# Kernel tuning notes

Hardware: AMD Instinct MI355X
Metric: run time of the kernel (lower is better)

The kernel has to match this reference:

```python
import jax, jax.numpy as jnp
from jax import lax
import numpy as np

N, C, D, KNN = 32768, 1000, 1024, 16
EPS_EUC = 1e-12
EPS_COS = 1e-8
COS_THRESH = 0.85


def setup_inputs() -> dict:
    key = jax.random.key(0)
    k1, k2, k3 = jax.random.split(key, 3)
    feature = jax.random.normal(k1, (N, D), dtype=jnp.float32)
    pred = jax.random.normal(k2, (N, C), dtype=jnp.float32)
    unlabeled_index = jnp.arange(N, dtype=jnp.int64) if jax.config.jax_enable_x64 else jnp.arange(N, dtype=jnp.int32)
    # module state: centroids (from FeaturePool), top-N score buffer (init -1), fake index buffer (init -1)
    centroids = jax.random.normal(k3, (C, D), dtype=jnp.float32)
    pred_top_N = jnp.full((C, KNN), -1.0, dtype=jnp.float32)
    fake_index = jnp.full((C, KNN), -1, dtype=jnp.int32)
    return {"feature": feature, "pred": pred, "unlabeled_index": unlabeled_index,
            "centroids": centroids, "pred_top_N": pred_top_N, "fake_index": fake_index}


def reference(feature, pred, unlabeled_index, centroids, pred_top_N, fake_index):
    xx = jnp.sum(feature * feature, axis=1, keepdims=True)          # [N,1]
    yy = jnp.sum(centroids * centroids, axis=1)[None, :]            # [1,C]
    euc = jnp.sqrt(jnp.clip(xx + yy - 2.0 * (feature @ centroids.T), EPS_EUC, None))
    euc_id = jnp.argmin(euc, axis=1)                                # [N]

    scores = jnp.max(jax.nn.softmax(pred, axis=1), axis=1)          # [N] max softmax prob

    # cosine similarity of every sample to every centroid [N, C]
    f_n = feature / jnp.clip(jnp.linalg.norm(feature, axis=1, keepdims=True), EPS_COS, None)
    c_n = centroids / jnp.clip(jnp.linalg.norm(centroids, axis=1, keepdims=True), EPS_COS, None)
    cos = f_n @ c_n.T
    label_idx = jnp.argmax(cos, axis=1)                             # [N]
    cos_max = jnp.max(cos, axis=1)                                  # [N]

    # label[i] = label_idx if (cos-argmax == euc-argmin and cos_max > 0.85) else -1
    label = jnp.where((label_idx == euc_id) & (cos_max > COS_THRESH),
                      label_idx.astype(jnp.float32), -1.0)

    # sequential bounded top-N scatter update of (pred_top_N, fake_index)
    def step(carry, x):
        ptn, fidx = carry
        li, sc, ui = x
        row = ptn[li]                        # [KNN]
        mi = jnp.argmin(row)
        upd = sc > row[mi]
        ptn = ptn.at[li, mi].set(jnp.where(upd, sc, row[mi]))
        fidx = fidx.at[li, mi].set(jnp.where(upd, ui.astype(fidx.dtype), fidx[li, mi]))
        return (ptn, fidx), None

    (ptn_new, fidx_new), _ = lax.scan(step, (pred_top_N, fake_index),
                                      (label_idx, scores, unlabeled_index))
    return label, ptn_new, fidx_new
```

## Files before the change

kernel.cpp:

```cpp
#include <hip/hip_runtime.h>
#include <hip/hip_bf16.h>
#include <math.h>

#define NS 32768
#define NC 1000
#define CP 1024
#define DD 1024
#define KN 16

typedef __attribute__((ext_vector_type(8))) short bf16x8;
typedef __attribute__((ext_vector_type(4))) float f32x4;
typedef __attribute__((ext_vector_type(4))) float float4v;
typedef __attribute__((ext_vector_type(4))) int int4v;
typedef __attribute__((ext_vector_type(8))) unsigned short u16x8;
typedef __attribute__((ext_vector_type(4))) unsigned short u16x4;

__device__ __forceinline__ unsigned short f2bf(float f) {
  unsigned u = __float_as_uint(f);
  u += 0x7FFFu + ((u >> 16) & 1u);
  return (unsigned short)(u >> 16);
}
__device__ __forceinline__ float bf2f(unsigned short h) {
  return __uint_as_float(((unsigned)h) << 16);
}

#define GLL16(g, l) __builtin_amdgcn_global_load_lds( \
    (const __attribute__((address_space(1))) void*)(g), \
    (__attribute__((address_space(3))) void*)(l), 16, 0, 0)

#define PREP_FEAT_BLKS (NS * DD / 4 / 1024)
__global__ __launch_bounds__(256) void k_prep(
    const float* __restrict__ Cm, unsigned short* __restrict__ Cb,
    float* __restrict__ cnorm2, float* __restrict__ invc,
    const float* __restrict__ A, unsigned short* __restrict__ Ab,
    const float* __restrict__ P, float* __restrict__ scores) {
  __shared__ float red[4];
  __shared__ float wmax[4];
  __shared__ double wsum[4];
  int b = blockIdx.x, tid = threadIdx.x;
  int lane = tid & 63, wid = tid >> 6;
  if (b < NS) {
    const float* row = P + (size_t)b * NC;
    bool act = tid < 250;
    float p0 = 0, p1 = 0, p2 = 0, p3 = 0, mx = -1e30f;
    if (act) {
      float4v v = *(const float4v*)(row + tid * 4);
      p0 = v[0]; p1 = v[1]; p2 = v[2]; p3 = v[3];
      mx = fmaxf(fmaxf(p0, p1), fmaxf(p2, p3));
    }
    for (int off = 32; off; off >>= 1) mx = fmaxf(mx, __shfl_xor(mx, off));
    if (!lane) wmax[wid] = mx;
    __syncthreads();
    float m = fmaxf(fmaxf(wmax[0], wmax[1]), fmaxf(wmax[2], wmax[3]));
    double s = 0.0;
    if (act)
      s = (double)__expf(p0 - m) + (double)__expf(p1 - m) +
          (double)__expf(p2 - m) + (double)__expf(p3 - m);
    for (int off = 32; off; off >>= 1) s += __shfl_xor(s, off);
    if (!lane) wsum[wid] = s;
    __syncthreads();
    if (!tid) scores[b] = (float)(1.0 / (wsum[0] + wsum[1] + wsum[2] + wsum[3]));
  } else if (b < NS + PREP_FEAT_BLKS) {
    int bb = b - NS;
    const float4v* src = (const float4v*)A;
    u16x4* dst = (u16x4*)Ab;
#pragma unroll
    for (int r = 0; r < 4; ++r) {
      size_t f = (size_t)bb * 1024 + r * 256 + tid;
      float4v v = src[f];
      u16x4 o = { f2bf(v[0]), f2bf(v[1]), f2bf(v[2]), f2bf(v[3]) };
      dst[f] = o;
    }
  } else {
    int c = b - NS - PREP_FEAT_BLKS;
    float sq = 0.f;
    if (c < NC) {
      float4v v = ((const float4v*)(Cm + (size_t)c * DD))[tid];
      sq = v[0]*v[0] + v[1]*v[1] + v[2]*v[2] + v[3]*v[3];
      u16x4 o = { f2bf(v[0]), f2bf(v[1]), f2bf(v[2]), f2bf(v[3]) };
      *(u16x4*)(Cb + (size_t)c * DD + tid * 4) = o;
    } else {
      u16x4 z = { 0, 0, 0, 0 };
      *(u16x4*)(Cb + (size_t)c * DD + tid * 4) = z;
    }
    for (int off = 32; off; off >>= 1) sq += __shfl_xor(sq, off);
    if (!lane) red[wid] = sq;
    __syncthreads();
    if (!tid) {
      float s = red[0] + red[1] + red[2] + red[3];
      cnorm2[c] = s;
      float n = sqrtf(s); if (n < 1e-8f) n = 1e-8f;
      invc[c] = (c < NC) ? 1.0f / n : 0.0f;
    }
  }
}

#define MF(a_, b_, c_) __builtin_amdgcn_mfma_f32_16x16x32_bf16(a_, b_, c_, 0, 0, 0)
#define RD(base_, i_) (*(const bf16x8*)((base_) + (i_) * 1024 + aoff))
#define SA(s_, b_) do { \
    GLL16(pA0 + (s_) * 32, ldsB + (b_) * 16384 + dA0); \
    GLL16(pA1 + (s_) * 32, ldsB + (b_) * 16384 + dA1); } while (0)
#define SB(s_, b_) do { \
    GLL16(pB0 + (s_) * 32, ldsB + 65536 + (b_) * 16384 + dA0); \
    GLL16(pB1 + (s_) * 32, ldsB + 65536 + (b_) * 16384 + dA1); } while (0)
#define VM4 asm volatile("s_waitcnt vmcnt(4)" ::: "memory")
#define VM0 asm volatile("s_waitcnt vmcnt(0)" ::: "memory")
#define MFMAC(A0_, A1_, A2_, A3_, M0) do { \
    acc[M0+0][0] = MF(A0_, bv0, acc[M0+0][0]); \
    acc[M0+0][1] = MF(A0_, bv1, acc[M0+0][1]); \
    acc[M0+0][2] = MF(A0_, bv2, acc[M0+0][2]); \
    acc[M0+0][3] = MF(A0_, bv3, acc[M0+0][3]); \
    acc[M0+1][0] = MF(A1_, bv0, acc[M0+1][0]); \
    acc[M0+1][1] = MF(A1_, bv1, acc[M0+1][1]); \
    acc[M0+1][2] = MF(A1_, bv2, acc[M0+1][2]); \
    acc[M0+1][3] = MF(A1_, bv3, acc[M0+1][3]); \
    acc[M0+2][0] = MF(A2_, bv0, acc[M0+2][0]); \
    acc[M0+2][1] = MF(A2_, bv1, acc[M0+2][1]); \
    acc[M0+2][2] = MF(A2_, bv2, acc[M0+2][2]); \
    acc[M0+2][3] = MF(A2_, bv3, acc[M0+2][3]); \
    acc[M0+3][0] = MF(A3_, bv0, acc[M0+3][0]); \
    acc[M0+3][1] = MF(A3_, bv1, acc[M0+3][1]); \
    acc[M0+3][2] = MF(A3_, bv2, acc[M0+3][2]); \
    acc[M0+3][3] = MF(A3_, bv3, acc[M0+3][3]); } while (0)
#define KSTEP(s_, STAGE_, GATE_) do { \
    const char* Ab_ = ldsB + ((s_) & 3) * 16384 + wrOff; \
    const char* Bb_ = ldsB + 65536 + ((s_) & 3) * 16384 + wcOff; \
    af0 = RD(Ab_, 0); af1 = RD(Ab_, 1); af2 = RD(Ab_, 2); af3 = RD(Ab_, 3); \
    bv0 = RD(Bb_, 0); bv1 = RD(Bb_, 1); bv2 = RD(Bb_, 2); bv3 = RD(Bb_, 3); \
    af4 = RD(Ab_, 4); af5 = RD(Ab_, 5); af6 = RD(Ab_, 6); af7 = RD(Ab_, 7); \
    STAGE_; \
    __builtin_amdgcn_s_setprio(1); \
    MFMAC(af0, af1, af2, af3, 0); \
    MFMAC(af4, af5, af6, af7, 4); \
    __builtin_amdgcn_s_setprio(0); \
    GATE_; \
    __builtin_amdgcn_s_barrier(); \
  } while (0)

__global__ __launch_bounds__(512, 1) void k_gemm(
    const unsigned short* __restrict__ A,
    const unsigned short* __restrict__ B,
    unsigned short* __restrict__ Dout) {
  __shared__ unsigned short lds[65536];
  char* ldsB = (char*)lds;
  int tid = threadIdx.x, lane = tid & 63, wid = tid >> 6;
  int wr = wid >> 2, wc = wid & 3;
  int bid = (blockIdx.x & 7) * 64 + (blockIdx.x >> 3);
  int cb = bid & 3, rb = bid >> 2;
  int brow = rb * 256, bcol = cb * 256;

  f32x4 acc[8][4];
#pragma unroll
  for (int m = 0; m < 8; ++m)
#pragma unroll
    for (int n = 0; n < 4; ++n) acc[m][n] = (f32x4){0.f, 0.f, 0.f, 0.f};

  int f0 = wid * 64 + lane, f1 = f0 + 512;
  int gl0 = (f0 & 3) ^ ((f0 >> 3) & 3);
  int gl1 = (f1 & 3) ^ ((f1 >> 3) & 3);
  const unsigned short* pA0 = A + (size_t)(brow + (f0 >> 2)) * DD + gl0 * 8;
  const unsigned short* pA1 = A + (size_t)(brow + (f1 >> 2)) * DD + gl1 * 8;
  const unsigned short* pB0 = B + (size_t)(bcol + (f0 >> 2)) * DD + gl0 * 8;
  const unsigned short* pB1 = B + (size_t)(bcol + (f1 >> 2)) * DD + gl1 * 8;
  int dA0 = f0 * 16, dA1 = f1 * 16;

  int aoff = (lane & 15) * 64 + (((lane >> 4) ^ ((lane >> 1) & 3)) * 16);
  int wrOff = wr * 8192;
  int wcOff = wc * 4096;

  bf16x8 af0, af1, af2, af3, af4, af5, af6, af7, bv0, bv1, bv2, bv3;

  SA(0, 0); SB(0, 0);
  SA(1, 1); SB(1, 1);
  VM4;
  __builtin_amdgcn_s_barrier();

  for (int s = 0; s < 30; ++s) {
    int bn = (s + 2) & 3;
    KSTEP(s, { SA(s + 2, bn); SB(s + 2, bn); }, VM4);
  }
  KSTEP(30, (void)0, VM0);
  KSTEP(31, (void)0, (void)0);

  int colb = bcol + wc * 64 + (lane & 15);
  int rowb = brow + wr * 128 + ((lane >> 4) << 2);
#pragma unroll
  for (int m = 0; m < 8; ++m)
#pragma unroll
    for (int n = 0; n < 4; ++n)
#pragma unroll
      for (int j = 0; j < 4; ++j)
        Dout[(size_t)(rowb + m * 16 + j) * CP + colb + n * 16] = f2bf(acc[m][n][j]);
}

__global__ __launch_bounds__(256) void k_argmax(
    const unsigned short* __restrict__ Dot, const float* __restrict__ invc,
    const float* __restrict__ cnorm2, const float* __restrict__ feat,
    const float* __restrict__ cent, float* __restrict__ label_out,
    int* __restrict__ lidx) {
  int tid = threadIdx.x;
  int lane = tid & 63, wid = tid >> 6;
  int i = blockIdx.x * 4 + wid;
  const unsigned short* drow = Dot + (size_t)i * CP;

  float v[2][8];
  float dmax = -1e30f; int darg = CP;
  float emin = 1e30f;  int earg = CP;
#pragma unroll
  for (int it = 0; it < 2; ++it) {
    int c0 = it * 512 + lane * 8;
    bf16x8 d8 = *(const bf16x8*)(drow + c0);
    float4v i0 = *(const float4v*)(invc + c0);
    float4v i1 = *(const float4v*)(invc + c0 + 4);
    float4v n0 = *(const float4v*)(cnorm2 + c0);
    float4v n1 = *(const float4v*)(cnorm2 + c0 + 4);
#pragma unroll
    for (int j = 0; j < 8; ++j) {
      int c = c0 + j;
      float inv = (j < 4) ? i0[j] : i1[j - 4];
      float cn  = (j < 4) ? n0[j] : n1[j - 4];
      float d = bf2f((unsigned short)d8[j]);
      float val, ev;
      if (c < NC) { val = d * inv; ev = cn - 2.0f * d; }
      else        { val = -1e30f;  ev = 1e30f; }
      v[it][j] = val;
      if (val > dmax) { dmax = val; darg = c; }
      if (ev < emin)  { emin = ev;  earg = c; }
    }
  }
  for (int off = 32; off; off >>= 1) {
    float om = __shfl_xor(dmax, off); int oi = __shfl_xor(darg, off);
    if (om > dmax || (om == dmax && oi < darg)) { dmax = om; darg = oi; }
    float oe = __shfl_xor(emin, off); int oj = __shfl_xor(earg, off);
    if (oe < emin || (oe == emin && oj < earg)) { emin = oe; earg = oj; }
  }
  const float MARGIN = 0.15f;
  unsigned long long cmask[2][8]; int ccnt = 0;
#pragma unroll
  for (int it = 0; it < 2; ++it)
#pragma unroll
    for (int j = 0; j < 8; ++j) {
      int c = it * 512 + lane * 8 + j;
      bool cand = (c < NC) && (v[it][j] >= dmax - MARGIN);
      cmask[it][j] = __ballot(cand);
      ccnt += __popcll(cmask[it][j]);
    }
  int finalArg = darg;
  double cosmax_d = -2.0;
  bool need = (ccnt > 1) || (dmax > 10.0f);
  if (need) {
    float xv[16]; double sx = 0.0;
    const float* xr = feat + (size_t)i * DD;
#pragma unroll
    for (int t = 0; t < 16; ++t) {
      float x = xr[t * 64 + lane]; xv[t] = x; sx += (double)x * (double)x;
    }
    for (int off = 32; off; off >>= 1) sx += __shfl_xor(sx, off);
    double nx = sqrt(sx); if (nx < 1e-8) nx = 1e-8;
    double best = -2.0; int besti = CP;
#pragma unroll
    for (int it = 0; it < 2; ++it)
#pragma unroll
      for (int j = 0; j < 8; ++j) {
        unsigned long long mk = cmask[it][j];
        while (mk) {
          int b = __builtin_ctzll(mk); mk &= mk - 1;
          int c = it * 512 + b * 8 + j;
          const float* cr = cent + (size_t)c * DD;
          double s = 0.0, s2 = 0.0;
#pragma unroll
          for (int t = 0; t < 16; ++t) {
            double cv = (double)cr[t * 64 + lane];
            s += (double)xv[t] * cv; s2 += cv * cv;
          }
          for (int off = 32; off; off >>= 1) {
            s += __shfl_xor(s, off); s2 += __shfl_xor(s2, off);
          }
          double nc = sqrt(s2); if (nc < 1e-8) nc = 1e-8;
          double cs = s / (nx * nc);
          if (cs > best || (cs == best && c < besti)) { best = cs; besti = c; }
        }
      }
    finalArg = besti; cosmax_d = best;
  }
  if (!lane) {
    lidx[i] = finalArg;
    float lab = -1.0f;
    if (need && finalArg == earg && cosmax_d > 0.85) lab = (float)finalArg;
    label_out[i] = lab;
  }
}

__global__ __launch_bounds__(64) void k_scan(
    const int* __restrict__ lidx, const float* __restrict__ scores,
    const int* __restrict__ uidx, const float* __restrict__ ptn_in,
    const int* __restrict__ fidx_in, float* __restrict__ out_ptn,
    float* __restrict__ out_fidx) {
  int c = blockIdx.x;
  int lane = threadIdx.x;
  float row[KN]; int idx[KN];
#pragma unroll
  for (int j = 0; j < KN; ++j) {
    row[j] = ptn_in[c * KN + j];
    idx[j] = fidx_in[c * KN + j];
  }
  for (int base = 0; base < NS; base += 256) {
    int l0 = lidx[base + lane];
    int l1 = lidx[base + 64 + lane];
    int l2 = lidx[base + 128 + lane];
    int l3 = lidx[base + 192 + lane];
#pragma unroll
    for (int q = 0; q < 4; ++q) {
      int lab = (q == 0) ? l0 : (q == 1) ? l1 : (q == 2) ? l2 : l3;
      unsigned long long m = __ballot(lab == c);
      while (m) {
        int b = __builtin_ctzll(m); m &= m - 1;
        int i = base + q * 64 + b;
        float s = scores[i];
        int ui = uidx[i];
        int mi = 0; float mn = row[0];
#pragma unroll
        for (int t = 1; t < KN; ++t)
          if (row[t] < mn) { mn = row[t]; mi = t; }
        if (s > mn) {
#pragma unroll
          for (int t = 0; t < KN; ++t)
            if (t == mi) { row[t] = s; idx[t] = ui; }
        }
      }
    }
  }
  if (!lane) {
#pragma unroll
    for (int j = 0; j < KN; ++j) {
      out_ptn[c * KN + j] = row[j];
      out_fidx[c * KN + j] = (float)idx[j];
    }
  }
}

extern "C" void kernel_launch(void* const* d_in, const int* in_sizes, int n_in,
                              void* d_out, int out_size, void* d_ws, size_t ws_size,
                              hipStream_t stream) {
  const float* feature = (const float*)d_in[0];
  const float* pred    = (const float*)d_in[1];
  const int*   uidx    = (const int*)d_in[2];
  const float* cent    = (const float*)d_in[3];
  const float* ptn_in  = (const float*)d_in[4];
  const int*   fidx_in = (const int*)d_in[5];
  float* out = (float*)d_out;

  char* ws = (char*)d_ws;
  unsigned short* cent_bf = (unsigned short*)(ws);
  unsigned short* feat_bf = (unsigned short*)(ws + (2ull << 20));
  unsigned short* dot_bf  = (unsigned short*)(ws + (66ull << 20));
  float* scores = (float*)(ws + (130ull << 20));
  int*   lidx   = (int*)  (ws + (130ull << 20) + (128ull << 10));
  float* cnorm2 = (float*)(ws + (130ull << 20) + (256ull << 10));
  float* invc   = (float*)(ws + (130ull << 20) + (260ull << 10));

  hipLaunchKernelGGL(k_prep, dim3(NS + PREP_FEAT_BLKS + CP), dim3(256), 0, stream,
                     cent, cent_bf, cnorm2, invc,
                     feature, feat_bf, pred, scores);
  hipLaunchKernelGGL(k_gemm, dim3((NS / 256) * (CP / 256)), dim3(512), 0, stream,
                     feat_bf, cent_bf, dot_bf);
  hipLaunchKernelGGL(k_argmax, dim3(NS / 4), dim3(256), 0, stream,
                     dot_bf, invc, cnorm2, feature, cent, out, lidx);
  hipLaunchKernelGGL(k_scan, dim3(NC), dim3(64), 0, stream,
                     lidx, scores, uidx, ptn_in, fidx_in,
                     out + NS, out + NS + NC * KN);
}
```

Before: 217.4 us.

## Fuse per-tile argmax/argmin reduction into GEMM epilogue, read partials in reduce

The GEMM epilogue now computes per-row cosine argmax and euclidean argmin over its 256-column tile, combining the four wave-columns through LDS and writing one float4 partial per row and column block. The follow-up kernel merges the four partials and only rereads the bf16 dot row for column blocks whose max falls within the margin, which cuts most of the full dot-matrix read. The dot matrix is still written in full, and the GEMM epilogue gains shuffles, an LDS pass and a barrier. The LDS reuse relies on the final k-step barrier so that pipeline buffers are no longer being read.

```diff
diff --git a/kernel.cpp b/kernel.cpp
--- a/kernel.cpp
+++ b/kernel.cpp
@@ -140,7 +140,9 @@
 __global__ __launch_bounds__(512, 1) void k_gemm(
     const unsigned short* __restrict__ A,
     const unsigned short* __restrict__ B,
-    unsigned short* __restrict__ Dout) {
+    unsigned short* __restrict__ Dout,
+    const float* __restrict__ invc, const float* __restrict__ cnorm2,
+    float4v* __restrict__ part) {
   __shared__ unsigned short lds[65536];
   char* ldsB = (char*)lds;
   int tid = threadIdx.x, lane = tid & 63, wid = tid >> 6;
@@ -182,8 +184,9 @@
   KSTEP(30, (void)0, VM0);
   KSTEP(31, (void)0, (void)0);
 
-  int colb = bcol + wc * 64 + (lane & 15);
-  int rowb = brow + wr * 128 + ((lane >> 4) << 2);
+  int lc = lane & 15, sub = lane >> 4;
+  int colb = bcol + wc * 64 + lc;
+  int rowb = brow + wr * 128 + (sub << 2);
 #pragma unroll
   for (int m = 0; m < 8; ++m)
 #pragma unroll
@@ -191,63 +194,105 @@
 #pragma unroll
       for (int j = 0; j < 4; ++j)
         Dout[(size_t)(rowb + m * 16 + j) * CP + colb + n * 16] = f2bf(acc[m][n][j]);
-}
-
-__global__ __launch_bounds__(256) void k_argmax(
-    const unsigned short* __restrict__ Dot, const float* __restrict__ invc,
-    const float* __restrict__ cnorm2, const float* __restrict__ feat,
+
+  float inv_n[4], cn_n[4]; int c_n[4];
+#pragma unroll
+  for (int n = 0; n < 4; ++n) {
+    c_n[n] = bcol + wc * 64 + n * 16 + lc;
+    inv_n[n] = invc[c_n[n]]; cn_n[n] = cnorm2[c_n[n]];
+  }
+  float4v* lp = (float4v*)ldsB;
+#pragma unroll
+  for (int m = 0; m < 8; ++m)
+#pragma unroll
+    for (int j = 0; j < 4; ++j) {
+      float vmax = -1e30f; int varg = CP;
+      float vemin = 1e30f; int vearg = CP;
+#pragma unroll
+      for (int n = 0; n < 4; ++n) {
+        float d = bf2f(f2bf(acc[m][n][j]));
+        float val, ev;
+        if (c_n[n] < NC) { val = d * inv_n[n]; ev = cn_n[n] - 2.0f * d; }
+        else             { val = -1e30f;       ev = 1e30f; }
+        if (val > vmax) { vmax = val; varg = c_n[n]; }
+        if (ev < vemin) { vemin = ev; vearg = c_n[n]; }
+      }
+#pragma unroll
+      for (int off = 1; off < 16; off <<= 1) {
+        float om = __shfl_xor(vmax, off); int oi = __shfl_xor(varg, off);
+        if (om > vmax || (om == vmax && oi < varg)) { vmax = om; varg = oi; }
+        float oe = __shfl_xor(vemin, off); int oj = __shfl_xor(vearg, off);
+        if (oe < vemin || (oe == vemin && oj < vearg)) { vemin = oe; vearg = oj; }
+      }
+      if (lc == 0) {
+        int row = wr * 128 + m * 16 + sub * 4 + j;
+        lp[row * 4 + wc] = (float4v){ vmax, __int_as_float(varg),
+                                      vemin, __int_as_float(vearg) };
+      }
+    }
+  __builtin_amdgcn_s_barrier();
+  if (tid < 256) {
+    int row = tid;
+    float4v p0 = lp[row * 4];
+    float bmax = p0[0]; int barg = __float_as_int(p0[1]);
+    float bemin = p0[2]; int bearg = __float_as_int(p0[3]);
+#pragma unroll
+    for (int w = 1; w < 4; ++w) {
+      float4v p = lp[row * 4 + w];
+      float m2 = p[0]; int a2 = __float_as_int(p[1]);
+      if (m2 > bmax || (m2 == bmax && a2 < barg)) { bmax = m2; barg = a2; }
+      float e2 = p[2]; int g2 = __float_as_int(p[3]);
+      if (e2 < bemin || (e2 == bemin && g2 < bearg)) { bemin = e2; bearg = g2; }
+    }
+    part[(size_t)(brow + row) * 4 + cb] =
+        (float4v){ bmax, __int_as_float(barg), bemin, __int_as_float(bearg) };
+  }
+}
+
+__global__ __launch_bounds__(256) void k_reduce(
+    const unsigned short* __restrict__ Dot, const float4v* __restrict__ part,
+    const float* __restrict__ invc, const float* __restrict__ feat,
     const float* __restrict__ cent, float* __restrict__ label_out,
     int* __restrict__ lidx) {
   int tid = threadIdx.x;
   int lane = tid & 63, wid = tid >> 6;
   int i = blockIdx.x * 4 + wid;
-  const unsigned short* drow = Dot + (size_t)i * CP;
-
-  float v[2][8];
-  float dmax = -1e30f; int darg = CP;
+
+  float bmax[4]; int barg[4];
+  float gmax = -1e30f; int garg = CP;
   float emin = 1e30f;  int earg = CP;
 #pragma unroll
-  for (int it = 0; it < 2; ++it) {
-    int c0 = it * 512 + lane * 8;
-    bf16x8 d8 = *(const bf16x8*)(drow + c0);
-    float4v i0 = *(const float4v*)(invc + c0);
-    float4v i1 = *(const float4v*)(invc + c0 + 4);
-    float4v n0 = *(const float4v*)(cnorm2 + c0);
-    float4v n1 = *(const float4v*)(cnorm2 + c0 + 4);
-#pragma unroll
-    for (int j = 0; j < 8; ++j) {
-      int c = c0 + j;
-      float inv = (j < 4) ? i0[j] : i1[j - 4];
-      float cn  = (j < 4) ? n0[j] : n1[j - 4];
-      float d = bf2f((unsigned short)d8[j]);
-      float val, ev;
-      if (c < NC) { val = d * inv; ev = cn - 2.0f * d; }
-      else        { val = -1e30f;  ev = 1e30f; }
-      v[it][j] = val;
-      if (val > dmax) { dmax = val; darg = c; }
-      if (ev < emin)  { emin = ev;  earg = c; }
-    }
-  }
-  for (int off = 32; off; off >>= 1) {
-    float om = __shfl_xor(dmax, off); int oi = __shfl_xor(darg, off);
-    if (om > dmax || (om == dmax && oi < darg)) { dmax = om; darg = oi; }
-    float oe = __shfl_xor(emin, off); int oj = __shfl_xor(earg, off);
-    if (oe < emin || (oe == emin && oj < earg)) { emin = oe; earg = oj; }
+  for (int j = 0; j < 4; ++j) {
+    float4v p = part[(size_t)i * 4 + j];
+    bmax[j] = p[0]; barg[j] = __float_as_int(p[1]);
+    if (p[0] > gmax || (p[0] == gmax && barg[j] < garg)) { gmax = p[0]; garg = barg[j]; }
+    float e = p[2]; int g = __float_as_int(p[3]);
+    if (e < emin || (e == emin && g < earg)) { emin = e; earg = g; }
   }
   const float MARGIN = 0.15f;
-  unsigned long long cmask[2][8]; int ccnt = 0;
-#pragma unroll
-  for (int it = 0; it < 2; ++it)
-#pragma unroll
-    for (int j = 0; j < 8; ++j) {
-      int c = it * 512 + lane * 8 + j;
-      bool cand = (c < NC) && (v[it][j] >= dmax - MARGIN);
-      cmask[it][j] = __ballot(cand);
-      ccnt += __popcll(cmask[it][j]);
-    }
-  int finalArg = darg;
+  unsigned long long cmask[4][4]; int ccnt = 0;
+#pragma unroll
+  for (int j = 0; j < 4; ++j) {
+    if (bmax[j] >= gmax - MARGIN) {
+      int c0 = j * 256 + lane * 4;
+      u16x4 d4 = *(const u16x4*)(Dot + (size_t)i * CP + c0);
+      float4v iv = *(const float4v*)(invc + c0);
+#pragma unroll
+      for (int t = 0; t < 4; ++t) {
+        int c = c0 + t;
+        float val = (c < NC) ? bf2f((unsigned short)d4[t]) * iv[t] : -1e30f;
+        bool cand = val >= gmax - MARGIN;
+        cmask[j][t] = __ballot(cand);
+        ccnt += __popcll(cmask[j][t]);
+      }
+    } else {
+#pragma unroll
+      for (int t = 0; t < 4; ++t) cmask[j][t] = 0ull;
+    }
+  }
+  int finalArg = garg;
   double cosmax_d = -2.0;
-  bool need = (ccnt > 1) || (dmax > 10.0f);
+  bool need = (ccnt > 1) || (gmax > 10.0f);
   if (need) {
     float xv[16]; double sx = 0.0;
     const float* xr = feat + (size_t)i * DD;
@@ -259,19 +304,19 @@
     double nx = sqrt(sx); if (nx < 1e-8) nx = 1e-8;
     double best = -2.0; int besti = CP;
 #pragma unroll
-    for (int it = 0; it < 2; ++it)
-#pragma unroll
-      for (int j = 0; j < 8; ++j) {
-        unsigned long long mk = cmask[it][j];
+    for (int j = 0; j < 4; ++j)
+#pragma unroll
+      for (int t = 0; t < 4; ++t) {
+        unsigned long long mk = cmask[j][t];
         while (mk) {
           int b = __builtin_ctzll(mk); mk &= mk - 1;
-          int c = it * 512 + b * 8 + j;
+          int c = j * 256 + b * 4 + t;
           const float* cr = cent + (size_t)c * DD;
           double s = 0.0, s2 = 0.0;
 #pragma unroll
-          for (int t = 0; t < 16; ++t) {
-            double cv = (double)cr[t * 64 + lane];
-            s += (double)xv[t] * cv; s2 += cv * cv;
+          for (int t2 = 0; t2 < 16; ++t2) {
+            double cv = (double)cr[t2 * 64 + lane];
+            s += (double)xv[t2] * cv; s2 += cv * cv;
           }
           for (int off = 32; off; off >>= 1) {
             s += __shfl_xor(s, off); s2 += __shfl_xor(s2, off);
@@ -358,14 +403,15 @@
   int*   lidx   = (int*)  (ws + (130ull << 20) + (128ull << 10));
   float* cnorm2 = (float*)(ws + (130ull << 20) + (256ull << 10));
   float* invc   = (float*)(ws + (130ull << 20) + (260ull << 10));
+  float4v* part = (float4v*)(ws + (131ull << 20));
 
   hipLaunchKernelGGL(k_prep, dim3(NS + PREP_FEAT_BLKS + CP), dim3(256), 0, stream,
                      cent, cent_bf, cnorm2, invc,
                      feature, feat_bf, pred, scores);
   hipLaunchKernelGGL(k_gemm, dim3((NS / 256) * (CP / 256)), dim3(512), 0, stream,
-                     feat_bf, cent_bf, dot_bf);
-  hipLaunchKernelGGL(k_argmax, dim3(NS / 4), dim3(256), 0, stream,
-                     dot_bf, invc, cnorm2, feature, cent, out, lidx);
+                     feat_bf, cent_bf, dot_bf, invc, cnorm2, part);
+  hipLaunchKernelGGL(k_reduce, dim3(NS / 4), dim3(256), 0, stream,
+                     dot_bf, part, invc, feature, cent, out, lidx);
   hipLaunchKernelGGL(k_scan, dim3(NC), dim3(64), 0, stream,
                      lidx, scores, uidx, ptn_in, fidx_in,
                      out + NS, out + NS + NC * KN);
```

Result: slower. 340.5 us (+56.7%).
